# Kernel optimization log

Hardware: AMD Instinct MI355X
Metric: run time of the kernel (lower is better)

The kernel has to match this reference:

```python
import jax, jax.numpy as jnp
import numpy as np

BETA = 5.5  # exp-cosine kernel sharpness (module default)

def _l2norm(x, axis=-1):
    return x / jnp.linalg.norm(x, axis=axis, keepdims=True)

def setup_inputs() -> dict:
    key = jax.random.key(0)
    ks = jax.random.split(key, 7)
    C, Mt, D = 1000, 33, 1024  # classes, memory slots (32 learned + 1 fixed), feat dim
    img_feat = jax.random.normal(ks[0], (1, D), jnp.float32)
    memory = jax.random.normal(ks[1], (C, Mt, D), jnp.float32)
    # simulate unfilled memory slots (exercises the zero-row masking branch)
    memory = memory.at[:, 24:32, :].set(0.0)
    global_bias = jax.random.normal(ks[2], (C, D), jnp.float32) * 0.02
    global_bias_key = jax.random.normal(ks[3], (C, D), jnp.float32) * 0.02
    global_bias_value = jax.random.normal(ks[4], (C, D), jnp.float32) * 0.02
    global_ffn_bias = jax.random.normal(ks[5], (C, D), jnp.float32) * 0.02
    logit_scale = jnp.ones((1,), jnp.float32) * jnp.log(100.0).astype(jnp.float32)
    return {
        "img_feat": img_feat,
        "memory": memory,
        "global_bias": global_bias,
        "global_bias_key": global_bias_key,
        "global_bias_value": global_bias_value,
        "global_ffn_bias": global_ffn_bias,
        "logit_scale": logit_scale,
    }

def reference(img_feat, memory, global_bias, global_bias_key, global_bias_value,
              global_ffn_bias, logit_scale):
    # position == 'all', center_type_clip == 'attn'
    # query: image feature shifted by mean class bias, L2-normalized
    q = _l2norm(img_feat + jnp.mean(global_bias, axis=0, keepdims=True))  # [1, D]
    # keys / values: per-class bias add + L2 norm, with empty slots zeroed
    empty = (jnp.sum(memory, axis=-1) == 0)[..., None]                    # [C, Mt, 1]
    K = jnp.where(empty, 0.0, _l2norm(memory + global_bias_key[:, None, :]))
    V = jnp.where(empty, 0.0, _l2norm(memory + global_bias_value[:, None, :]))
    # exp-cosine similarity kernel: exp(-beta * (1 - cos))
    sim = jnp.einsum('d,cmd->cm', q[0], K)                                # [C, Mt]
    sim = jnp.exp(-BETA * (1.0 - sim))
    # weighted sum over memory slots, renormalize, output bias, renormalize
    a = _l2norm(jnp.einsum('cm,cmd->cd', sim, V))                          # [C, D]
    a = _l2norm(a + global_ffn_bias)
    logits = jnp.exp(logit_scale[0]) * (a @ img_feat[0])                   # [C]
    return jax.nn.softmax(logits)[None, :]                                 # [1, C]
```

## Files before the change

kernel.cpp:

```cpp
#include <hip/hip_runtime.h>
#include <math.h>

#define NCLS 1000
#define MT 33
#define D 1024
#define BETA 5.5f

__device__ __forceinline__ float wave_sum(float v) {
#pragma unroll
  for (int off = 32; off; off >>= 1) v += __shfl_xor(v, off, 64);
  return v;
}

__device__ __forceinline__ float dot4(float4 a, float4 b) {
  return a.x * b.x + a.y * b.y + a.z * b.z + a.w * b.w;
}
__device__ __forceinline__ float sum4(float4 a) { return a.x + a.y + a.z + a.w; }

__device__ __forceinline__ float block_sum16(float v, volatile float* scr) {
  v = wave_sum(v);
  const int wv = threadIdx.x >> 6, lane = threadIdx.x & 63;
  if (lane == 0) scr[wv] = v;
  __syncthreads();
  if (wv == 0) {
    float x = (lane < 16) ? scr[lane] : 0.0f;
#pragma unroll
    for (int off = 8; off; off >>= 1) x += __shfl_xor(x, off, 64);
    if (lane == 0) scr[16] = x;
  }
  __syncthreads();
  return scr[16];
}

__global__ __launch_bounds__(1024) void zero_kernel(float* __restrict__ s) {
  s[threadIdx.x] = 0.0f;
}

__global__ __launch_bounds__(1024) void colsum_kernel(const float* __restrict__ gb,
                                                      float* __restrict__ s) {
  const int t = threadIdx.x;
  float p = 0.0f;
  for (int c = blockIdx.x; c < NCLS; c += gridDim.x) p += gb[(size_t)c * D + t];
  atomicAdd(&s[t], p);
}

__global__ __launch_bounds__(1024) void qnorm_kernel(const float* __restrict__ img,
                                                     const float* __restrict__ s,
                                                     float* __restrict__ q) {
  __shared__ float scr[17];
  const int t = threadIdx.x;
  const float v = img[t] + s[t] * (1.0f / (float)NCLS);
  const float ss = block_sum16(v * v, scr);
  q[t] = v / sqrtf(ss);
}

__global__ __launch_bounds__(1024) void main_kernel(
    const float* __restrict__ memp, const float* __restrict__ gbk,
    const float* __restrict__ gbv, const float* __restrict__ gffn,
    const float* __restrict__ img, const float* __restrict__ qvec,
    const float* __restrict__ ls, float* __restrict__ logits) {
  __shared__ float red[8 * D];
  __shared__ float scr[17];
  const int c = blockIdx.x;
  const int t = threadIdx.x;
  const int wv = t >> 6, lane = t & 63;
  const int dbase = lane * 4;

  const float* gbk_c = gbk + (size_t)c * D;
  const float* gbv_c = gbv + (size_t)c * D;

  float4 qv[4], kv[4], vvr[4];
#pragma unroll
  for (int k = 0; k < 4; ++k) {
    const int d = k * 256 + dbase;
    qv[k] = *(const float4*)(qvec + d);
    kv[k] = *(const float4*)(gbk_c + d);
    vvr[k] = *(const float4*)(gbv_c + d);
  }
  float kk = 0.0f, vv2 = 0.0f, qk = 0.0f;
#pragma unroll
  for (int k = 0; k < 4; ++k) {
    kk += dot4(kv[k], kv[k]);
    vv2 += dot4(vvr[k], vvr[k]);
    qk += dot4(qv[k], kv[k]);
  }
  kk = wave_sum(kk);
  vv2 = wave_sum(vv2);
  qk = wave_sum(qk);

  float4 acc[4];
#pragma unroll
  for (int k = 0; k < 4; ++k) acc[k] = make_float4(0.f, 0.f, 0.f, 0.f);
  float Wsum = 0.0f;

  const float* memc = memp + (size_t)c * MT * D;
  for (int m = wv; m < MT; m += 16) {
    float4 mv[4];
#pragma unroll
    for (int k = 0; k < 4; ++k)
      mv[k] = *(const float4*)(memc + (size_t)m * D + k * 256 + dbase);
    float pqm = 0.f, pkm = 0.f, pvm = 0.f, pmm = 0.f, ps = 0.f;
#pragma unroll
    for (int k = 0; k < 4; ++k) {
      pqm += dot4(qv[k], mv[k]);
      pkm += dot4(kv[k], mv[k]);
      pvm += dot4(vvr[k], mv[k]);
      pmm += dot4(mv[k], mv[k]);
      ps += sum4(mv[k]);
    }
    pqm = wave_sum(pqm);
    pkm = wave_sum(pkm);
    pvm = wave_sum(pvm);
    pmm = wave_sum(pmm);
    ps = wave_sum(ps);

    const float nk = sqrtf(pmm + 2.0f * pkm + kk);
    const float cosv = (pqm + qk) / nk;
    const float sim = expf(-BETA * (1.0f - cosv));
    const float nv = sqrtf(pmm + 2.0f * pvm + vv2);
    const float wgt = (ps == 0.0f) ? 0.0f : sim / nv;
    Wsum += wgt;
#pragma unroll
    for (int k = 0; k < 4; ++k) {
      acc[k].x += wgt * mv[k].x;
      acc[k].y += wgt * mv[k].y;
      acc[k].z += wgt * mv[k].z;
      acc[k].w += wgt * mv[k].w;
    }
  }
#pragma unroll
  for (int k = 0; k < 4; ++k) {
    acc[k].x += Wsum * vvr[k].x;
    acc[k].y += Wsum * vvr[k].y;
    acc[k].z += Wsum * vvr[k].z;
    acc[k].w += Wsum * vvr[k].w;
  }

#pragma unroll
  for (int half = 8; half >= 1; half >>= 1) {
    if (wv >= half && wv < 2 * half) {
      float* dst = red + (wv - half) * D + dbase;
#pragma unroll
      for (int k = 0; k < 4; ++k) *(float4*)(dst + k * 256) = acc[k];
    }
    __syncthreads();
    if (wv < half) {
      const float* src = red + wv * D + dbase;
#pragma unroll
      for (int k = 0; k < 4; ++k) {
        const float4 t4 = *(const float4*)(src + k * 256);
        acc[k].x += t4.x;
        acc[k].y += t4.y;
        acc[k].z += t4.z;
        acc[k].w += t4.w;
      }
    }
    __syncthreads();
  }
  if (wv == 0) {
#pragma unroll
    for (int k = 0; k < 4; ++k) *(float4*)(red + k * 256 + dbase) = acc[k];
  }
  __syncthreads();

  const float araw = red[t];
  const float n1sq = block_sum16(araw * araw, scr);
  const float a1 = araw / sqrtf(n1sq) + gffn[(size_t)c * D + t];
  const float n2sq = block_sum16(a1 * a1, scr);
  const float d3 = block_sum16(a1 * img[t], scr);
  if (t == 0) logits[c] = expf(ls[0]) * d3 / sqrtf(n2sq);
}

__global__ __launch_bounds__(1024) void softmax_kernel(const float* __restrict__ logits,
                                                       float* __restrict__ out) {
  __shared__ float scr[17];
  const int t = threadIdx.x;
  const int wv = t >> 6, lane = t & 63;
  const float l = (t < NCLS) ? logits[t] : -INFINITY;
  float m = l;
#pragma unroll
  for (int off = 32; off; off >>= 1) m = fmaxf(m, __shfl_xor(m, off, 64));
  if (lane == 0) scr[wv] = m;
  __syncthreads();
  if (wv == 0) {
    float x = (lane < 16) ? scr[lane] : -INFINITY;
#pragma unroll
    for (int off = 8; off; off >>= 1) x = fmaxf(x, __shfl_xor(x, off, 64));
    if (lane == 0) scr[16] = x;
  }
  __syncthreads();
  m = scr[16];
  const float e = (t < NCLS) ? expf(l - m) : 0.0f;
  const float s = block_sum16(e, scr);
  if (t < NCLS) out[t] = e / s;
}

extern "C" void kernel_launch(void* const* d_in, const int* in_sizes, int n_in,
                              void* d_out, int out_size, void* d_ws, size_t ws_size,
                              hipStream_t stream) {
  const float* img = (const float*)d_in[0];
  const float* memp = (const float*)d_in[1];
  const float* gb = (const float*)d_in[2];
  const float* gbk = (const float*)d_in[3];
  const float* gbv = (const float*)d_in[4];
  const float* gffn = (const float*)d_in[5];
  const float* ls = (const float*)d_in[6];
  float* out = (float*)d_out;

  float* s = (float*)d_ws;
  float* q = s + D;
  float* logits = q + D;

  zero_kernel<<<1, D, 0, stream>>>(s);
  colsum_kernel<<<64, D, 0, stream>>>(gb, s);
  qnorm_kernel<<<1, D, 0, stream>>>(img, s, q);
  main_kernel<<<NCLS, D, 0, stream>>>(memp, gbk, gbv, gffn, img, q, ls, logits);
  softmax_kernel<<<1, D, 0, stream>>>(logits, out);
}
```

Before: 241.6 us.

## Fuse query normalization into main kernel and flatten block reductions

```diff
diff --git a/kernel.cpp b/kernel.cpp
--- a/kernel.cpp
+++ b/kernel.cpp
@@ -15,7 +15,6 @@
 __device__ __forceinline__ float dot4(float4 a, float4 b) {
   return a.x * b.x + a.y * b.y + a.z * b.z + a.w * b.w;
 }
-__device__ __forceinline__ float sum4(float4 a) { return a.x + a.y + a.z + a.w; }
 
 __device__ __forceinline__ float block_sum16(float v, volatile float* scr) {
   v = wave_sum(v);
@@ -30,6 +29,32 @@
   }
   __syncthreads();
   return scr[16];
+}
+
+__device__ __forceinline__ float2 block_sum2(float a, float b, volatile float* scr) {
+  a = wave_sum(a);
+  b = wave_sum(b);
+  const int wv = threadIdx.x >> 6, lane = threadIdx.x & 63;
+  if (lane == 0) {
+    scr[wv] = a;
+    scr[16 + wv] = b;
+  }
+  __syncthreads();
+  if (wv == 0) {
+    float x = (lane < 16) ? scr[lane] : 0.0f;
+    float y = (lane < 16) ? scr[16 + lane] : 0.0f;
+#pragma unroll
+    for (int off = 8; off; off >>= 1) {
+      x += __shfl_xor(x, off, 64);
+      y += __shfl_xor(y, off, 64);
+    }
+    if (lane == 0) {
+      scr[32] = x;
+      scr[33] = y;
+    }
+  }
+  __syncthreads();
+  return make_float2(scr[32], scr[33]);
 }
 
 __global__ __launch_bounds__(1024) void zero_kernel(float* __restrict__ s) {
@@ -44,23 +69,13 @@
   atomicAdd(&s[t], p);
 }
 
-__global__ __launch_bounds__(1024) void qnorm_kernel(const float* __restrict__ img,
-                                                     const float* __restrict__ s,
-                                                     float* __restrict__ q) {
-  __shared__ float scr[17];
-  const int t = threadIdx.x;
-  const float v = img[t] + s[t] * (1.0f / (float)NCLS);
-  const float ss = block_sum16(v * v, scr);
-  q[t] = v / sqrtf(ss);
-}
-
 __global__ __launch_bounds__(1024) void main_kernel(
     const float* __restrict__ memp, const float* __restrict__ gbk,
     const float* __restrict__ gbv, const float* __restrict__ gffn,
-    const float* __restrict__ img, const float* __restrict__ qvec,
+    const float* __restrict__ img, const float* __restrict__ s,
     const float* __restrict__ ls, float* __restrict__ logits) {
   __shared__ float red[8 * D];
-  __shared__ float scr[17];
+  __shared__ float scr[40];
   const int c = blockIdx.x;
   const int t = threadIdx.x;
   const int wv = t >> 6, lane = t & 63;
@@ -70,13 +85,29 @@
   const float* gbv_c = gbv + (size_t)c * D;
 
   float4 qv[4], kv[4], vvr[4];
+  float qss = 0.0f;
 #pragma unroll
   for (int k = 0; k < 4; ++k) {
     const int d = k * 256 + dbase;
-    qv[k] = *(const float4*)(qvec + d);
+    const float4 iv = *(const float4*)(img + d);
+    const float4 sv = *(const float4*)(s + d);
+    float4 v;
+    v.x = iv.x + sv.x * (1.0f / (float)NCLS);
+    v.y = iv.y + sv.y * (1.0f / (float)NCLS);
+    v.z = iv.z + sv.z * (1.0f / (float)NCLS);
+    v.w = iv.w + sv.w * (1.0f / (float)NCLS);
+    qv[k] = v;
+    qss += dot4(v, v);
     kv[k] = *(const float4*)(gbk_c + d);
     vvr[k] = *(const float4*)(gbv_c + d);
   }
+  qss = wave_sum(qss);
+  const float qinv = 1.0f / sqrtf(qss);
+#pragma unroll
+  for (int k = 0; k < 4; ++k) {
+    qv[k].x *= qinv; qv[k].y *= qinv; qv[k].z *= qinv; qv[k].w *= qinv;
+  }
+
   float kk = 0.0f, vv2 = 0.0f, qk = 0.0f;
 #pragma unroll
   for (int k = 0; k < 4; ++k) {
@@ -99,26 +130,24 @@
 #pragma unroll
     for (int k = 0; k < 4; ++k)
       mv[k] = *(const float4*)(memc + (size_t)m * D + k * 256 + dbase);
-    float pqm = 0.f, pkm = 0.f, pvm = 0.f, pmm = 0.f, ps = 0.f;
+    float pqm = 0.f, pkm = 0.f, pvm = 0.f, pmm = 0.f;
 #pragma unroll
     for (int k = 0; k < 4; ++k) {
       pqm += dot4(qv[k], mv[k]);
       pkm += dot4(kv[k], mv[k]);
       pvm += dot4(vvr[k], mv[k]);
       pmm += dot4(mv[k], mv[k]);
-      ps += sum4(mv[k]);
     }
     pqm = wave_sum(pqm);
     pkm = wave_sum(pkm);
     pvm = wave_sum(pvm);
     pmm = wave_sum(pmm);
-    ps = wave_sum(ps);
 
     const float nk = sqrtf(pmm + 2.0f * pkm + kk);
     const float cosv = (pqm + qk) / nk;
     const float sim = expf(-BETA * (1.0f - cosv));
     const float nv = sqrtf(pmm + 2.0f * pvm + vv2);
-    const float wgt = (ps == 0.0f) ? 0.0f : sim / nv;
+    const float wgt = (pmm == 0.0f) ? 0.0f : sim / nv;
     Wsum += wgt;
 #pragma unroll
     for (int k = 0; k < 4; ++k) {
@@ -136,44 +165,39 @@
     acc[k].w += Wsum * vvr[k].w;
   }
 
-#pragma unroll
-  for (int half = 8; half >= 1; half >>= 1) {
-    if (wv >= half && wv < 2 * half) {
-      float* dst = red + (wv - half) * D + dbase;
-#pragma unroll
-      for (int k = 0; k < 4; ++k) *(float4*)(dst + k * 256) = acc[k];
-    }
-    __syncthreads();
-    if (wv < half) {
-      const float* src = red + wv * D + dbase;
-#pragma unroll
-      for (int k = 0; k < 4; ++k) {
-        const float4 t4 = *(const float4*)(src + k * 256);
-        acc[k].x += t4.x;
-        acc[k].y += t4.y;
-        acc[k].z += t4.z;
-        acc[k].w += t4.w;
-      }
-    }
-    __syncthreads();
-  }
-  if (wv == 0) {
-#pragma unroll
-    for (int k = 0; k < 4; ++k) *(float4*)(red + k * 256 + dbase) = acc[k];
-  }
-  __syncthreads();
-
-  const float araw = red[t];
+  if (wv >= 8) {
+    float* dst = red + (wv - 8) * D + dbase;
+#pragma unroll
+    for (int k = 0; k < 4; ++k) *(float4*)(dst + k * 256) = acc[k];
+  }
+  __syncthreads();
+  if (wv < 8) {
+    float* ptr = red + wv * D + dbase;
+#pragma unroll
+    for (int k = 0; k < 4; ++k) {
+      const float4 t4 = *(const float4*)(ptr + k * 256);
+      acc[k].x += t4.x;
+      acc[k].y += t4.y;
+      acc[k].z += t4.z;
+      acc[k].w += t4.w;
+    }
+#pragma unroll
+    for (int k = 0; k < 4; ++k) *(float4*)(ptr + k * 256) = acc[k];
+  }
+  __syncthreads();
+  float araw = 0.0f;
+#pragma unroll
+  for (int w = 0; w < 8; ++w) araw += red[w * D + t];
+
   const float n1sq = block_sum16(araw * araw, scr);
   const float a1 = araw / sqrtf(n1sq) + gffn[(size_t)c * D + t];
-  const float n2sq = block_sum16(a1 * a1, scr);
-  const float d3 = block_sum16(a1 * img[t], scr);
-  if (t == 0) logits[c] = expf(ls[0]) * d3 / sqrtf(n2sq);
+  const float2 r2 = block_sum2(a1 * a1, a1 * img[t], scr);
+  if (t == 0) logits[c] = expf(ls[0]) * r2.y / sqrtf(r2.x);
 }
 
 __global__ __launch_bounds__(1024) void softmax_kernel(const float* __restrict__ logits,
                                                        float* __restrict__ out) {
-  __shared__ float scr[17];
+  __shared__ float scr[40];
   const int t = threadIdx.x;
   const int wv = t >> 6, lane = t & 63;
   const float l = (t < NCLS) ? logits[t] : -INFINITY;
@@ -191,8 +215,8 @@
   __syncthreads();
   m = scr[16];
   const float e = (t < NCLS) ? expf(l - m) : 0.0f;
-  const float s = block_sum16(e, scr);
-  if (t < NCLS) out[t] = e / s;
+  const float sden = block_sum16(e, scr);
+  if (t < NCLS) out[t] = e / sden;
 }
 
 extern "C" void kernel_launch(void* const* d_in, const int* in_sizes, int n_in,
@@ -208,12 +232,10 @@
   float* out = (float*)d_out;
 
   float* s = (float*)d_ws;
-  float* q = s + D;
-  float* logits = q + D;
+  float* logits = s + D;
 
   zero_kernel<<<1, D, 0, stream>>>(s);
   colsum_kernel<<<64, D, 0, stream>>>(gb, s);
-  qnorm_kernel<<<1, D, 0, stream>>>(img, s, q);
-  main_kernel<<<NCLS, D, 0, stream>>>(memp, gbk, gbv, gffn, img, q, ls, logits);
+  main_kernel<<<NCLS, D, 0, stream>>>(memp, gbk, gbv, gffn, img, s, ls, logits);
   softmax_kernel<<<1, D, 0, stream>>>(logits, out);
 }
```

Result: no change. 237.0 us (-1.9%).
